# Performance work log

Measured on AMD Instinct MI355X. Metric: run time of the kernel, lower is better.

Reference implementation:

```python
import jax, jax.numpy as jnp
import numpy as np

MIN_VAL = 0.0
MAX_VAL = 1.0
NUM_BINS = 512
NUM_NODES = 128
GRAD_SMOOTH = 0.01
BIN_W = (MAX_VAL - MIN_VAL) / NUM_BINS


def _make_kernels():
    sobel = jnp.array([-1.0, 0.0, 1.0], dtype=jnp.float32) / (2.0 * BIN_W)
    r = max(1, int(GRAD_SMOOTH / BIN_W))  # kernel radius in bins
    idx = jnp.arange(2 * r + 1, dtype=jnp.float32) - r
    sigma = GRAD_SMOOTH / BIN_W
    g = jnp.exp(-0.5 * (idx / sigma) ** 2)
    return sobel, g / jnp.sum(g)


def _conv1d_reflect(x, k):
    # x: [N, B], k: [K]; torch Conv1d = cross-correlation with reflect padding
    pad = (k.shape[0] - 1) // 2
    xp = jnp.pad(x, ((0, 0), (pad, pad)), mode='reflect')
    out = jax.lax.conv_general_dilated(
        xp[:, None, :], k[None, None, :], (1,), 'VALID',
        dimension_numbers=('NCH', 'OIH', 'NCH'))
    return out[:, 0, :]


def _compute_cdf_pdf(residuals, weights, src_indices, dst_indices):
    # histogram bin per sample (floor)
    bi = jnp.floor((residuals - MIN_VAL) / BIN_W).astype(jnp.int32)
    valid = (bi >= 0) & (bi < NUM_BINS)
    bi = jnp.clip(bi, 0, NUM_BINS - 1)
    wc = (weights * valid).reshape(-1)  # [N_pairs*K]

    src_comb = (src_indices[:, None] * NUM_BINS + bi).reshape(-1)
    dst_comb = (dst_indices[:, None] * NUM_BINS + bi).reshape(-1)
    nseg = NUM_NODES * NUM_BINS
    hist = (jax.ops.segment_sum(wc, src_comb, num_segments=nseg)
            + jax.ops.segment_sum(wc, dst_comb, num_segments=nseg))
    hist = hist.reshape(NUM_NODES, NUM_BINS)

    wflat = weights.reshape(-1)
    src_exp = jnp.broadcast_to(src_indices[:, None], residuals.shape).reshape(-1)
    dst_exp = jnp.broadcast_to(dst_indices[:, None], residuals.shape).reshape(-1)
    tw = (jax.ops.segment_sum(wflat, src_exp, num_segments=NUM_NODES)
          + jax.ops.segment_sum(wflat, dst_exp, num_segments=NUM_NODES))

    pmf = hist / (tw[:, None] + 1e-10)
    cdf = jnp.cumsum(pmf, axis=1)
    sobel, gauss = _make_kernels()
    pdf = _conv1d_reflect(_conv1d_reflect(cdf, sobel), gauss)
    return cdf, pdf


def _lookup(residuals, weights, cdf, pdf, src_indices, dst_indices):
    # rounded bin for lookup (floor of x + 0.5)
    bi = jnp.floor((residuals - MIN_VAL) / BIN_W + 0.5).astype(jnp.int32)
    valid = (bi >= 0) & (bi < NUM_BINS) & (weights > 0.0)
    bi = jnp.clip(bi, 0, NUM_BINS - 1)
    src_cdf = cdf[src_indices[:, None], bi]
    dst_cdf = cdf[dst_indices[:, None], bi]
    src_grad = pdf[src_indices[:, None], bi] * weights
    dst_grad = pdf[dst_indices[:, None], bi] * weights
    two = jnp.float32(2.0)
    return (jnp.where(valid, src_cdf, two),
            jnp.where(valid, src_grad, 0.0),
            jnp.where(valid, dst_cdf, two),
            jnp.where(valid, dst_grad, 0.0))


def setup_inputs() -> dict:
    key = jax.random.key(0)
    k1, k2, k3, k4 = jax.random.split(key, 4)
    N_pairs, K = 1024, 16384
    return {
        'residuals': jax.random.uniform(k1, (N_pairs, K), dtype=jnp.float32),
        'weights': jax.random.uniform(k2, (N_pairs, K), dtype=jnp.float32),
        'src_indices': jax.random.randint(k3, (N_pairs,), 0, NUM_NODES),
        'dst_indices': jax.random.randint(k4, (N_pairs,), 0, NUM_NODES),
    }


def reference(residuals, weights, src_indices, dst_indices):
    cdf, pdf = _compute_cdf_pdf(residuals, weights, src_indices, dst_indices)
    src_cdf, _, dst_cdf, _ = _lookup(residuals, weights, cdf, pdf,
                                     src_indices, dst_indices)
    return src_cdf, dst_cdf
```

## Files before the change

kernel.cpp:

```cpp
#include <hip/hip_runtime.h>

#define NUM_BINS  512
#define NUM_NODES 128
#define K_ELEMS   16384
#define N_PAIRS   1024
#define NCOPY     32

typedef float f32x4 __attribute__((ext_vector_type(4)));
typedef float f32x2 __attribute__((ext_vector_type(2)));
typedef unsigned int   u32;
typedef unsigned short u16;

__device__ __forceinline__ void gfadd(float* p, float v) { unsafeAtomicAdd(p, v); }

__global__ __launch_bounds__(256) void zero_ws_kernel(float* __restrict__ ws, int n)
{
    int i = blockIdx.x * 256 + threadIdx.x;
    if (i < n) ws[i] = 0.0f;
}

__global__ __launch_bounds__(1024) void hist_kernel(
    const float* __restrict__ residuals, const float* __restrict__ weights,
    const int* __restrict__ src, const int* __restrict__ dst,
    float* __restrict__ hist, float* __restrict__ tw,
    u16* __restrict__ codes)
{
    __shared__ u32 lh[NUM_BINS * NCOPY];
    __shared__ float swsum[16];
    const int row  = blockIdx.x;
    const int t    = threadIdx.x;
    const int copy = t & 31;

    uint4* lh4 = (uint4*)lh;
    #pragma unroll
    for (int k = 0; k < NUM_BINS * NCOPY / 4 / 1024; ++k) {
        uint4 z; z.x = z.y = z.z = z.w = 0u;
        lh4[t + k * 1024] = z;
    }
    __syncthreads();

    const f32x4* r4 = (const f32x4*)(residuals + (size_t)row * K_ELEMS);
    const f32x4* w4 = (const f32x4*)(weights   + (size_t)row * K_ELEMS);
    ushort4*     c4 = (ushort4*)(codes + (size_t)row * K_ELEMS);

    float wsum = 0.0f;
    #pragma unroll
    for (int it = 0; it < K_ELEMS / 4 / 1024; ++it) {
        f32x4 r = __builtin_nontemporal_load(r4 + (t + it * 1024));
        f32x4 w = __builtin_nontemporal_load(w4 + (t + it * 1024));
        wsum += w[0] + w[1] + w[2] + w[3];
        ushort4 cv;
        u16* cp = (u16*)&cv;
        #pragma unroll
        for (int c = 0; c < 4; ++c) {
            int b = (int)floorf(r[c] * 512.0f);
            if ((unsigned)b < 512u)
                atomicAdd(&lh[b * NCOPY + copy], (u32)fmaf(w[c], 65536.0f, 0.5f));
            int lb = (int)floorf(r[c] * 512.0f + 0.5f);
            cp[c] = (u16)((((unsigned)lb < 512u) & (w[c] > 0.0f)) ? lb : 0xFFFF);
        }
        c4[t + it * 1024] = cv;
    }

    #pragma unroll
    for (int off = 32; off > 0; off >>= 1) wsum += __shfl_down(wsum, off, 64);
    const int wave = t >> 6, lane = t & 63;
    if (lane == 0) swsum[wave] = wsum;
    __syncthreads();

    const int s = src[row], d = dst[row];
    if (t == 0) {
        float tot = 0.0f;
        #pragma unroll
        for (int i = 0; i < 16; ++i) tot += swsum[i];
        gfadd(&tw[s], tot);
        gfadd(&tw[d], tot);
    }

    {
        const int bin  = t >> 1;
        const int half = t & 1;
        u32 tot = 0;
        #pragma unroll
        for (int cc = 0; cc < 16; ++cc)
            tot += lh[bin * NCOPY + (((bin + cc) & 15) | (half << 4))];
        tot += (u32)__shfl_xor((int)tot, 1);
        float v = (float)tot * (1.0f / 65536.0f);
        if (half == 0) gfadd(&hist[s * NUM_BINS + bin], v);
        else           gfadd(&hist[d * NUM_BINS + bin], v);
    }
}

__global__ __launch_bounds__(512) void lookup_scan_kernel(
    const u16* __restrict__ codes,
    const int* __restrict__ src, const int* __restrict__ dst,
    const float* __restrict__ hist, const float* __restrict__ tw,
    float* __restrict__ out_src, float* __restrict__ out_dst)
{
    __shared__ f32x2 sd[NUM_BINS];
    const int row = blockIdx.x;
    const int t   = threadIdx.x;

    const int s = src[row], d = dst[row];
    {
        f32x2 v;
        v[0] = hist[s * NUM_BINS + t] / (tw[s] + 1e-10f);
        v[1] = hist[d * NUM_BINS + t] / (tw[d] + 1e-10f);
        sd[t] = v;
    }
    __syncthreads();

    for (int off = 1; off < NUM_BINS; off <<= 1) {
        f32x2 add = (t >= off) ? sd[t - off] : (f32x2){0.0f, 0.0f};
        __syncthreads();
        sd[t] += add;
        __syncthreads();
    }

    const size_t base = (size_t)row * K_ELEMS;
    const ushort4* c4 = (const ushort4*)(codes + base);
    f32x4*        os4 = (f32x4*)(out_src + base);
    f32x4*        od4 = (f32x4*)(out_dst + base);

    #pragma unroll
    for (int it = 0; it < K_ELEMS / 4 / 512; ++it) {
        ushort4 c = c4[t + it * 512];
        f32x4 osv, odv;
        {   f32x2 v = (c.x != 0xFFFF) ? sd[c.x] : (f32x2){2.0f, 2.0f};
            osv[0] = v[0]; odv[0] = v[1]; }
        {   f32x2 v = (c.y != 0xFFFF) ? sd[c.y] : (f32x2){2.0f, 2.0f};
            osv[1] = v[0]; odv[1] = v[1]; }
        {   f32x2 v = (c.z != 0xFFFF) ? sd[c.z] : (f32x2){2.0f, 2.0f};
            osv[2] = v[0]; odv[2] = v[1]; }
        {   f32x2 v = (c.w != 0xFFFF) ? sd[c.w] : (f32x2){2.0f, 2.0f};
            osv[3] = v[0]; odv[3] = v[1]; }
        __builtin_nontemporal_store(osv, os4 + (t + it * 512));
        __builtin_nontemporal_store(odv, od4 + (t + it * 512));
    }
}

extern "C" void kernel_launch(void* const* d_in, const int* in_sizes, int n_in,
                              void* d_out, int out_size, void* d_ws, size_t ws_size,
                              hipStream_t stream)
{
    const float* residuals = (const float*)d_in[0];
    const float* weights   = (const float*)d_in[1];
    const int*   src       = (const int*)d_in[2];
    const int*   dst       = (const int*)d_in[3];

    float* out_src = (float*)d_out;
    float* out_dst = out_src + (size_t)N_PAIRS * K_ELEMS;

    float* hist  = (float*)d_ws;
    float* tw    = hist + NUM_NODES * NUM_BINS;
    u16*   codes = (u16*)((char*)d_ws + (4u << 20));

    const int ws_elems = NUM_NODES * NUM_BINS + NUM_NODES;
    zero_ws_kernel<<<(ws_elems + 255) / 256, 256, 0, stream>>>((float*)d_ws, ws_elems);

    hist_kernel<<<N_PAIRS, 1024, 0, stream>>>(residuals, weights, src, dst,
                                              hist, tw, codes);

    lookup_scan_kernel<<<N_PAIRS, 512, 0, stream>>>(codes, src, dst, hist, tw,
                                                    out_src, out_dst);
}
```

Measured before the change: 68.03 us.

## Replace per-element bin codes with validity bitmask and recompute bins from residuals

The histogram kernel no longer writes a 16-bit lookup bin per element. It writes a 16-bit validity mask per thread, and the lookup kernel rereads the residuals to recompute the rounded bin. Residual loads in the first kernel become regular (cacheable) loads so the second read may hit in the large last-level cache. This trades a 32MB write and read of codes for a 64MB reread of residuals plus a small mask, betting on cache reuse.

```diff
diff --git a/kernel.cpp b/kernel.cpp
--- a/kernel.cpp
+++ b/kernel.cpp
@@ -23,7 +23,7 @@
     const float* __restrict__ residuals, const float* __restrict__ weights,
     const int* __restrict__ src, const int* __restrict__ dst,
     float* __restrict__ hist, float* __restrict__ tw,
-    u16* __restrict__ codes)
+    u16* __restrict__ mask)
 {
     __shared__ u32 lh[NUM_BINS * NCOPY];
     __shared__ float swsum[16];
@@ -41,26 +41,25 @@
 
     const f32x4* r4 = (const f32x4*)(residuals + (size_t)row * K_ELEMS);
     const f32x4* w4 = (const f32x4*)(weights   + (size_t)row * K_ELEMS);
-    ushort4*     c4 = (ushort4*)(codes + (size_t)row * K_ELEMS);
 
     float wsum = 0.0f;
+    u32 vbits = 0;
     #pragma unroll
     for (int it = 0; it < K_ELEMS / 4 / 1024; ++it) {
-        f32x4 r = __builtin_nontemporal_load(r4 + (t + it * 1024));
+        f32x4 r = r4[t + it * 1024];
         f32x4 w = __builtin_nontemporal_load(w4 + (t + it * 1024));
         wsum += w[0] + w[1] + w[2] + w[3];
-        ushort4 cv;
-        u16* cp = (u16*)&cv;
         #pragma unroll
         for (int c = 0; c < 4; ++c) {
             int b = (int)floorf(r[c] * 512.0f);
             if ((unsigned)b < 512u)
                 atomicAdd(&lh[b * NCOPY + copy], (u32)fmaf(w[c], 65536.0f, 0.5f));
             int lb = (int)floorf(r[c] * 512.0f + 0.5f);
-            cp[c] = (u16)((((unsigned)lb < 512u) & (w[c] > 0.0f)) ? lb : 0xFFFF);
+            if (((unsigned)lb < 512u) & (w[c] > 0.0f))
+                vbits |= 1u << (it * 4 + c);
         }
-        c4[t + it * 1024] = cv;
     }
+    mask[(size_t)row * 1024 + t] = (u16)vbits;
 
     #pragma unroll
     for (int off = 32; off > 0; off >>= 1) wsum += __shfl_down(wsum, off, 64);
@@ -92,7 +91,7 @@
 }
 
 __global__ __launch_bounds__(512) void lookup_scan_kernel(
-    const u16* __restrict__ codes,
+    const float* __restrict__ residuals, const u16* __restrict__ mask,
     const int* __restrict__ src, const int* __restrict__ dst,
     const float* __restrict__ hist, const float* __restrict__ tw,
     float* __restrict__ out_src, float* __restrict__ out_dst)
@@ -118,24 +117,30 @@
     }
 
     const size_t base = (size_t)row * K_ELEMS;
-    const ushort4* c4 = (const ushort4*)(codes + base);
-    f32x4*        os4 = (f32x4*)(out_src + base);
-    f32x4*        od4 = (f32x4*)(out_dst + base);
+    const f32x4* r4   = (const f32x4*)(residuals + base);
+    f32x4*       os4  = (f32x4*)(out_src + base);
+    f32x4*       od4  = (f32x4*)(out_dst + base);
+
+    const u32 m0 = mask[(size_t)row * 1024 + t];
+    const u32 m1 = mask[(size_t)row * 1024 + t + 512];
 
     #pragma unroll
     for (int it = 0; it < K_ELEMS / 4 / 512; ++it) {
-        ushort4 c = c4[t + it * 512];
+        const int q = t + it * 512;
+        const u32 mw = (it & 1) ? m1 : m0;
+        const int kb = (it >> 1) * 4;
+        f32x4 r = r4[q];
         f32x4 osv, odv;
-        {   f32x2 v = (c.x != 0xFFFF) ? sd[c.x] : (f32x2){2.0f, 2.0f};
-            osv[0] = v[0]; odv[0] = v[1]; }
-        {   f32x2 v = (c.y != 0xFFFF) ? sd[c.y] : (f32x2){2.0f, 2.0f};
-            osv[1] = v[0]; odv[1] = v[1]; }
-        {   f32x2 v = (c.z != 0xFFFF) ? sd[c.z] : (f32x2){2.0f, 2.0f};
-            osv[2] = v[0]; odv[2] = v[1]; }
-        {   f32x2 v = (c.w != 0xFFFF) ? sd[c.w] : (f32x2){2.0f, 2.0f};
-            osv[3] = v[0]; odv[3] = v[1]; }
-        __builtin_nontemporal_store(osv, os4 + (t + it * 512));
-        __builtin_nontemporal_store(odv, od4 + (t + it * 512));
+        #pragma unroll
+        for (int c = 0; c < 4; ++c) {
+            int lb = (int)floorf(r[c] * 512.0f + 0.5f);
+            int bc = min(max(lb, 0), NUM_BINS - 1);
+            bool v = (mw >> (kb + c)) & 1u;
+            f32x2 vv = v ? sd[bc] : (f32x2){2.0f, 2.0f};
+            osv[c] = vv[0]; odv[c] = vv[1];
+        }
+        __builtin_nontemporal_store(osv, os4 + q);
+        __builtin_nontemporal_store(odv, od4 + q);
     }
 }
 
@@ -151,16 +156,16 @@
     float* out_src = (float*)d_out;
     float* out_dst = out_src + (size_t)N_PAIRS * K_ELEMS;
 
-    float* hist  = (float*)d_ws;
-    float* tw    = hist + NUM_NODES * NUM_BINS;
-    u16*   codes = (u16*)((char*)d_ws + (4u << 20));
+    float* hist = (float*)d_ws;
+    float* tw   = hist + NUM_NODES * NUM_BINS;
+    u16*   mask = (u16*)((char*)d_ws + (4u << 20));
 
     const int ws_elems = NUM_NODES * NUM_BINS + NUM_NODES;
     zero_ws_kernel<<<(ws_elems + 255) / 256, 256, 0, stream>>>((float*)d_ws, ws_elems);
 
     hist_kernel<<<N_PAIRS, 1024, 0, stream>>>(residuals, weights, src, dst,
-                                              hist, tw, codes);
+                                              hist, tw, mask);
 
-    lookup_scan_kernel<<<N_PAIRS, 512, 0, stream>>>(codes, src, dst, hist, tw,
-                                                    out_src, out_dst);
+    lookup_scan_kernel<<<N_PAIRS, 512, 0, stream>>>(residuals, mask, src, dst,
+                                                    hist, tw, out_src, out_dst);
 }
```

Result: faster. 66.68 us (-2.0%).
